# Kernel tuning notes

Measured on AMD Instinct MI355X. Metric: run time of the kernel, lower is better.

## Reference

```python
import jax, jax.numpy as jnp
import numpy as np


def setup_inputs() -> dict:
    key = jax.random.key(0)
    k1, k2, k3 = jax.random.split(key, 3)
    x = jax.random.normal(k1, (16, 64, 256, 256), dtype=jnp.float32)
    conv_weight = jax.random.normal(k2, (128, 64, 3, 3), dtype=jnp.float32) * 0.05
    conv_bias = jax.random.normal(k3, (128,), dtype=jnp.float32) * 0.05
    return {"x": x, "conv_weight": conv_weight, "conv_bias": conv_bias}


def reference(x, conv_weight, conv_bias):
    # Conv2d: stride 1, padding 0, dilation 1, groups 1 -> [B, out_c, 254, 254]
    y = jax.lax.conv_general_dilated(
        x, conv_weight,
        window_strides=(1, 1),
        padding="VALID",
        dimension_numbers=("NCHW", "OIHW", "NCHW"),
    ) + conv_bias[None, :, None, None]
    # Min over output channels (keepdim), then double tanh -> [B, 1, 254, 254]
    m = jnp.min(y, axis=1, keepdims=True)
    return jnp.tanh(jnp.tanh(m))
```

## Files before the change

kernel.cpp:

```cpp
#include <hip/hip_runtime.h>
#include <math.h>


typedef __attribute__((ext_vector_type(8))) short bf16x8;
typedef __attribute__((ext_vector_type(16))) float f32x16;

static __device__ __forceinline__ short f2bf(float f) {
    unsigned u = __float_as_uint(f);
    u += 0x7fffu + ((u >> 16) & 1u);
    return (short)(u >> 16);
}

__global__ void wtrans(const float* __restrict__ wg, short* __restrict__ wsB) {
    int o4 = blockIdx.x * 256 + threadIdx.x;
    if (o4 >= 18432) return;
    float4 v = ((const float4*)wg)[o4];
    float f[4] = {v.x, v.y, v.z, v.w};
    int base = o4 * 4;
    #pragma unroll
    for (int q = 0; q < 4; ++q) {
        int e  = base + q;
        int kw = e % 3, r1 = e / 3;
        int kh = r1 % 3, r2 = r1 / 3;
        int ic = r2 & 63, oc = r2 >> 6;
        int tap = kh * 3 + kw;
        int icc = ic >> 4, hi = (ic >> 3) & 1, j = ic & 7;
        int kstep = tap * 4 + icc;
        wsB[((kstep * 2 + hi) * 128 + oc) * 8 + j] = f2bf(f[q]);
    }
}

__global__ __launch_bounds__(256, 4)
void conv_min_tanh_mfma(const float* __restrict__ xg,
                        const short* __restrict__ wsB,
                        const float* __restrict__ bg,
                        float* __restrict__ out) {
    __shared__ __align__(16) short xt[16896];

    const int tid  = threadIdx.x;
    const int lane = tid & 63, l31 = lane & 31, hi = lane >> 5;
    const int w    = tid >> 6;
    const int r    = w & 1;
    const int nh   = w >> 1;
    const int ow0  = blockIdx.x * 64;
    const int oh0  = blockIdx.y * 2;
    const int b    = blockIdx.z;

    #pragma unroll
    for (int t = 0; t < 9; ++t) {
        int idx = t * 256 + tid;
        if (idx < 2112) {
            int g   = idx / 66;
            int col = idx - g * 66;
            int row = g >> 3;
            int icb = ((g >> 1) & 3) * 16 + (g & 1) * 8;
            int iw  = ow0 + col;
            const float* src = xg + (((size_t)(b * 64 + icb) * 256) + (oh0 + row)) * 256 + iw;
            bool valid = iw < 256;
            float f[8];
            #pragma unroll
            for (int j = 0; j < 8; ++j) f[j] = valid ? src[j * 65536] : 0.f;
            bf16x8 v;
            #pragma unroll
            for (int j = 0; j < 8; ++j) v[j] = f2bf(f[j]);
            *(bf16x8*)(xt + g * 528 + col * 8) = v;
        }
    }
    __syncthreads();

    f32x16 acc00 = {}, acc01 = {}, acc10 = {}, acc11 = {};

    const bf16x8* bp = (const bf16x8*)(wsB + ((size_t)hi * 128 + nh * 64 + l31) * 8);
    bf16x8 bc0 = bp[0], bc1 = bp[32];
    bf16x8 bn0 = bc0, bn1 = bc1;

    #pragma unroll
    for (int k = 0; k < 36; ++k) {
        if (k < 35) {
            bn0 = bp[(k + 1) * 256];
            bn1 = bp[(k + 1) * 256 + 32];
        }
        const int tap = k >> 2, icc = k & 3;
        const int kh = tap / 3, kw = tap - kh * 3;
        const bf16x8* ap = (const bf16x8*)(xt +
            (((r + kh) * 4 + icc) * 2 + hi) * 528 + (l31 + kw) * 8);
        bf16x8 a0 = ap[0];
        bf16x8 a1 = ap[32];
        acc00 = __builtin_amdgcn_mfma_f32_32x32x16_bf16(a0, bc0, acc00, 0, 0, 0);
        acc01 = __builtin_amdgcn_mfma_f32_32x32x16_bf16(a0, bc1, acc01, 0, 0, 0);
        acc10 = __builtin_amdgcn_mfma_f32_32x32x16_bf16(a1, bc0, acc10, 0, 0, 0);
        acc11 = __builtin_amdgcn_mfma_f32_32x32x16_bf16(a1, bc1, acc11, 0, 0, 0);
        bc0 = bn0; bc1 = bn1;
    }

    __syncthreads();
    float* sm = (float*)xt;
    const float bv0 = bg[nh * 64 + l31];
    const float bv1 = bg[nh * 64 + 32 + l31];
    #pragma unroll
    for (int reg = 0; reg < 16; ++reg) {
        const int m = (reg & 3) + 8 * (reg >> 2) + 4 * hi;
        float p0 = fminf(acc00[reg] + bv0, acc01[reg] + bv1);
        float p1 = fminf(acc10[reg] + bv0, acc11[reg] + bv1);
        sm[(r * 64 + m) * 65 + nh * 32 + l31]      = p0;
        sm[(r * 64 + 32 + m) * 65 + nh * 32 + l31] = p1;
    }
    __syncthreads();
    {
        const int px = tid >> 1, half = tid & 1;
        const float* rowp = sm + px * 65 + half * 32;
        float v = rowp[0];
        #pragma unroll
        for (int j = 1; j < 32; ++j) v = fminf(v, rowp[j]);
        v = fminf(v, __shfl_xor(v, 1, 64));
        if (half == 0) {
            v = tanhf(tanhf(v));
            const int ow = ow0 + (px & 63);
            const int oh = oh0 + (px >> 6);
            if (ow < 254)
                out[((size_t)b * 254 + oh) * 254 + ow] = v;
        }
    }
}

extern "C" void kernel_launch(void* const* d_in, const int* in_sizes, int n_in,
                              void* d_out, int out_size, void* d_ws, size_t ws_size,
                              hipStream_t stream) {
    const float* x  = (const float*)d_in[0];
    const float* wg = (const float*)d_in[1];
    const float* bs = (const float*)d_in[2];
    float* out = (float*)d_out;
    short* wsB = (short*)d_ws;

    wtrans<<<72, 256, 0, stream>>>(wg, wsB);
    dim3 grid(4, 127, 16);
    conv_min_tanh_mfma<<<grid, 256, 0, stream>>>(x, wsB, bs, out);
}
```

Baseline: 487.8 us.

## Deepen register prefetch of weights and LDS tiles in MFMA conv loop

The weight fragment prefetch goes from one k-step ahead to two, and the first two weight loads are issued before the barrier so they overlap the input staging. The LDS A-fragment loads are software-pipelined one k-step ahead of the MFMAs. Launch bounds drop from 4 to 3 waves per SIMD to give room for the extra live registers, which risks lower occupancy and less latency hiding across waves.

```diff
diff --git a/kernel.cpp b/kernel.cpp
--- a/kernel.cpp
+++ b/kernel.cpp
@@ -30,7 +30,7 @@
     }
 }
 
-__global__ __launch_bounds__(256, 4)
+__global__ __launch_bounds__(256, 3)
 void conv_min_tanh_mfma(const float* __restrict__ xg,
                         const short* __restrict__ wsB,
                         const float* __restrict__ bg,
@@ -66,31 +66,42 @@
             *(bf16x8*)(xt + g * 528 + col * 8) = v;
         }
     }
+
+    const bf16x8* bbase = (const bf16x8*)(wsB + ((size_t)hi * 128 + nh * 64 + l31) * 8);
+
+    bf16x8 bc0 = bbase[0],   bc1 = bbase[32];
+    bf16x8 bd0 = bbase[256], bd1 = bbase[256 + 32];
+    bf16x8 be0 = bd0, be1 = bd1;
+
     __syncthreads();
 
     f32x16 acc00 = {}, acc01 = {}, acc10 = {}, acc11 = {};
 
-    const bf16x8* bp = (const bf16x8*)(wsB + ((size_t)hi * 128 + nh * 64 + l31) * 8);
-    bf16x8 bc0 = bp[0], bc1 = bp[32];
-    bf16x8 bn0 = bc0, bn1 = bc1;
+    const bf16x8* ap0 = (const bf16x8*)(xt + ((r * 4 + 0) * 2 + hi) * 528 + l31 * 8);
+    bf16x8 a0 = ap0[0], a1 = ap0[32];
 
     #pragma unroll
     for (int k = 0; k < 36; ++k) {
+        if (k < 34) {
+            be0 = bbase[(k + 2) * 256];
+            be1 = bbase[(k + 2) * 256 + 32];
+        }
+        bf16x8 an0 = a0, an1 = a1;
         if (k < 35) {
-            bn0 = bp[(k + 1) * 256];
-            bn1 = bp[(k + 1) * 256 + 32];
+            const int kn = k + 1, tapn = kn >> 2, iccn = kn & 3;
+            const int khn = tapn / 3, kwn = tapn - khn * 3;
+            const bf16x8* apn = (const bf16x8*)(xt +
+                (((r + khn) * 4 + iccn) * 2 + hi) * 528 + (l31 + kwn) * 8);
+            an0 = apn[0];
+            an1 = apn[32];
         }
-        const int tap = k >> 2, icc = k & 3;
-        const int kh = tap / 3, kw = tap - kh * 3;
-        const bf16x8* ap = (const bf16x8*)(xt +
-            (((r + kh) * 4 + icc) * 2 + hi) * 528 + (l31 + kw) * 8);
-        bf16x8 a0 = ap[0];
-        bf16x8 a1 = ap[32];
         acc00 = __builtin_amdgcn_mfma_f32_32x32x16_bf16(a0, bc0, acc00, 0, 0, 0);
         acc01 = __builtin_amdgcn_mfma_f32_32x32x16_bf16(a0, bc1, acc01, 0, 0, 0);
         acc10 = __builtin_amdgcn_mfma_f32_32x32x16_bf16(a1, bc0, acc10, 0, 0, 0);
         acc11 = __builtin_amdgcn_mfma_f32_32x32x16_bf16(a1, bc1, acc11, 0, 0, 0);
-        bc0 = bn0; bc1 = bn1;
+        a0 = an0; a1 = an1;
+        bc0 = bd0; bc1 = bd1;
+        bd0 = be0; bd1 = be1;
     }
 
     __syncthreads();
```

After: 486.2 us. About the same (-0.3%).
